# Kernel optimization log

Hardware: AMD Instinct MI355X
Metric: run time of the kernel (lower is better)

Reference implementation:

```python
import jax, jax.numpy as jnp
import numpy as np

B, C, H, W = 2, 256, 100, 100
G, P = 4, 8
CG = C // G  # 64 per-group channels
EPS = 1e-5


def setup_inputs() -> dict:
    key = jax.random.key(0)
    ks = jax.random.split(key, 5)
    bev_query = jax.random.normal(ks[0], (B, C, H, W), dtype=jnp.float32)
    pts = jax.random.normal(ks[1], (B, H * W, 1, P, C), dtype=jnp.float32)
    conv_w = jax.random.normal(ks[2], (G * CG * CG, C), dtype=jnp.float32) * (1.0 / np.sqrt(C))
    conv_b = jax.random.normal(ks[3], (G * CG * CG,), dtype=jnp.float32) * 0.02
    ln_g = jnp.ones((CG,), dtype=jnp.float32)
    ln_b = jnp.zeros((CG,), dtype=jnp.float32)
    proj_w = jax.random.normal(ks[4], (CG, CG * P), dtype=jnp.float32) * (1.0 / np.sqrt(CG * P))
    proj_b = jnp.zeros((CG,), dtype=jnp.float32)
    return {"bev_query": bev_query, "pts": pts, "conv_w": conv_w, "conv_b": conv_b,
            "ln_g": ln_g, "ln_b": ln_b, "proj_w": proj_w, "proj_b": proj_b}


def reference(bev_query, pts, conv_w, conv_b, ln_g, ln_b, proj_w, proj_b):
    b, c, h, w = bev_query.shape
    q = h * w
    # pts: b q 1 p c -> b q p c
    pts = jnp.squeeze(pts, axis=2)
    # 1x1 conv parameter generator: b c h w -> b (g c1 c2) h w
    param = jnp.einsum('bchw,oc->bohw', bev_query, conv_w) + conv_b[None, :, None, None]
    # 'b (g c1 c2) h w -> (b g) (h w) c1 c2'
    param = param.reshape(b, G, CG, CG, q).transpose(0, 1, 4, 2, 3).reshape(b * G, q, CG, CG)
    # 'b q p (g c) -> (b g) q p c'
    pts_g = pts.reshape(b, q, P, G, CG).transpose(0, 3, 1, 2, 4).reshape(b * G, q, P, CG)
    # batched per-pixel matmul: (bg,q,p,c1) @ (bg,q,c1,c2) -> (bg,q,p,c2)
    mixed = jnp.matmul(pts_g, param)
    # LayerNorm over last dim + ReLU
    mu = jnp.mean(mixed, axis=-1, keepdims=True)
    var = jnp.var(mixed, axis=-1, keepdims=True)
    normed = (mixed - mu) * jax.lax.rsqrt(var + EPS) * ln_g + ln_b
    act = jax.nn.relu(normed)
    # 'b q p c -> b q (p c)' then linear
    flat = act.reshape(b * G, q, P * CG)
    out = jnp.einsum('bqi,oi->bqo', flat, proj_w) + proj_b
    # '(b g) (h w) c -> b (g c) h w'
    out = out.reshape(b, G, q, CG).transpose(0, 1, 3, 2).reshape(b, G * CG, h, w)
    return out
```

## Files before the change

### kernel.cpp

```cpp
#include <hip/hip_runtime.h>
#include <hip/hip_bf16.h>
#include <stdint.h>

#define QTOT 10000
#define MPAD 10240
#define CDIM 256
#define ODIM 16384
#define RTOT 20096

using f32x4  = __attribute__((ext_vector_type(4))) float;
using bf16x8 = __attribute__((ext_vector_type(8))) short;

#define GLOAD_LDS(gp, lp) __builtin_amdgcn_global_load_lds(                     \
    (const __attribute__((address_space(1))) unsigned int*)(gp),                \
    (__attribute__((address_space(3))) unsigned int*)(lp), 16, 0, 0)

static __device__ __forceinline__ short f2bs(float x) {
  __hip_bfloat16 h = __float2bfloat16(x);
  return *(short*)&h;
}

__global__ void cvt_f32_bf16(const float* __restrict__ s, __hip_bfloat16* __restrict__ d, int n) {
  for (int i = blockIdx.x * blockDim.x + threadIdx.x; i < n; i += gridDim.x * blockDim.x)
    d[i] = __float2bfloat16(s[i]);
}

__global__ void cvt_permute_cw(const float* __restrict__ s, __hip_bfloat16* __restrict__ d, int n) {
  for (int i = blockIdx.x * blockDim.x + threadIdx.x; i < n; i += gridDim.x * blockDim.x) {
    int rn = i >> 8, c = i & 255;
    int ro = (rn & ~4095) | ((rn & 63) << 6) | ((rn >> 6) & 63);
    d[i] = __float2bfloat16(s[ro * 256 + c]);
  }
}

__global__ __launch_bounds__(256) void transpose_bev(const float* __restrict__ bev,
                                                     __hip_bfloat16* __restrict__ bevT) {
  __shared__ float tl[32][33];
  int tx = threadIdx.x, ty = threadIdx.y;
  int q0 = blockIdx.x * 32, c0 = blockIdx.y * 32, b = blockIdx.z;
#pragma unroll
  for (int i = 0; i < 4; ++i) {
    int c = c0 + ty + i * 8, q = q0 + tx;
    tl[ty + i * 8][tx] = (q < QTOT) ? bev[((size_t)b * CDIM + c) * QTOT + q] : 0.0f;
  }
  __syncthreads();
#pragma unroll
  for (int i = 0; i < 4; ++i) {
    int q = q0 + ty + i * 8, c = c0 + tx;
    bevT[((size_t)b * MPAD + q) * CDIM + c] = __float2bfloat16(tl[tx][ty + i * 8]);
  }
}

__global__ __launch_bounds__(256) void gemm_param(const __hip_bfloat16* __restrict__ A,
                                                  const __hip_bfloat16* __restrict__ Bw,
                                                  const float* __restrict__ convb,
                                                  __hip_bfloat16* __restrict__ P,
                                                  int nbm) {
  __shared__ __align__(16) unsigned char smem[65536];
  int t = threadIdx.x, lane = t & 63, w = t >> 6;
  int id = blockIdx.x + nbm * blockIdx.y;
  int total = nbm * gridDim.y;
  int nid = (total & 7) ? id : ((id & 7) * (total >> 3) + (id >> 3));
  int bm = nid % nbm, bn = nid / nbm;
  int wm = (w >> 1) * 64, wn = (w & 1) * 64;
  int l15 = lane & 15, hi = lane >> 4;
  int srow = lane >> 3;
  int kbs  = ((lane & 7) ^ srow) * 8;
  const __hip_bfloat16* pA = A  + (size_t)(bm * 128 + w * 32 + srow) * CDIM + kbs;
  const __hip_bfloat16* pB = Bw + (size_t)(bn * 128 + w * 32 + srow) * CDIM + kbs;
  f32x4 acc[4][4] = {};

#define LSA(buf) (smem + (buf) * 16384)
#define LSB(buf) (smem + 32768 + (buf) * 16384)
#define STAGE_P(buf, kt) do {                                                   \
    _Pragma("unroll")                                                           \
    for (int i = 0; i < 4; ++i) {                                               \
      GLOAD_LDS(pA + (size_t)i * 8 * CDIM + (kt), LSA(buf) + (w * 4 + i) * 1024); \
      GLOAD_LDS(pB + (size_t)i * 8 * CDIM + (kt), LSB(buf) + (w * 4 + i) * 1024); \
    } } while (0)

  STAGE_P(0, 0);
  asm volatile("s_waitcnt vmcnt(0)" ::: "memory");
  __builtin_amdgcn_s_barrier();
#pragma unroll
  for (int kt = 0; kt < 4; ++kt) {
    const int cur = kt & 1;
    if (kt < 3) STAGE_P(cur ^ 1, (kt + 1) * 64);
    __builtin_amdgcn_sched_barrier(0);
#pragma unroll
    for (int kk = 0; kk < 2; ++kk) {
      int kb = kk * 64 + (hi << 4);
      bf16x8 af[4], bfr[4];
#pragma unroll
      for (int mi = 0; mi < 4; ++mi) {
        int row = wm + mi * 16 + l15;
        af[mi] = *(const bf16x8*)(LSA(cur) + ((row * 128 + kb) ^ ((row & 7) << 4)));
      }
#pragma unroll
      for (int ni = 0; ni < 4; ++ni) {
        int row = wn + ni * 16 + l15;
        bfr[ni] = *(const bf16x8*)(LSB(cur) + ((row * 128 + kb) ^ ((row & 7) << 4)));
      }
#pragma unroll
      for (int mi = 0; mi < 4; ++mi)
#pragma unroll
        for (int ni = 0; ni < 4; ++ni)
          acc[mi][ni] = __builtin_amdgcn_mfma_f32_16x16x32_bf16(af[mi], bfr[ni], acc[mi][ni], 0, 0, 0);
    }
    __builtin_amdgcn_sched_barrier(0);
    if (kt < 3) asm volatile("s_waitcnt vmcnt(0)" ::: "memory");
    __builtin_amdgcn_s_barrier();
    __builtin_amdgcn_sched_barrier(0);
  }
  short* st = (short*)smem;
#pragma unroll
  for (int ni = 0; ni < 4; ++ni) {
    int colL = wn + ni * 16 + l15;
    int col  = bn * 128 + colL;
    int o_old = (col & ~4095) | ((col & 63) << 6) | ((col >> 6) & 63);
    float cb = convb[o_old];
#pragma unroll
    for (int mi = 0; mi < 4; ++mi) {
      int rowL = wm + mi * 16 + hi * 4;
#pragma unroll
      for (int r = 0; r < 4; ++r)
        st[(rowL + r) * 136 + colL] = f2bs(acc[mi][ni][r] + cb);
    }
  }
  __syncthreads();
  {
    int cb8  = (t & 15) * 8;
    size_t colg = bn * 128 + cb8;
    size_t rb0  = (size_t)bm * 128;
#pragma unroll
    for (int it = 0; it < 8; ++it) {
      int row = it * 16 + (t >> 4);
      uint4 v = *(const uint4*)(st + row * 136 + cb8);
      *(uint4*)(P + (rb0 + row) * ODIM + colg) = v;
    }
  }
#undef STAGE_P
#undef LSA
#undef LSB
}

__global__ __launch_bounds__(256) void mix_mfma(const __hip_bfloat16* __restrict__ P,
                                                const float* __restrict__ pts,
                                                const float* __restrict__ lng,
                                                const float* __restrict__ lnb,
                                                __hip_bfloat16* __restrict__ act,
                                                int b, int q0) {
  __shared__ __align__(16) float ptsl[8 * 264];
  int t = threadIdx.x, lane = t & 63, g = t >> 6;
  int row = blockIdx.x;
  size_t rq = (size_t)b * QTOT + q0 + row;
  {
    const float4* ps = (const float4*)(pts + rq * 2048);
#pragma unroll
    for (int i = 0; i < 2; ++i) {
      int v = i * 256 + t;
      float4 val = ps[v];
      int p = v >> 6, c = (v & 63) * 4;
      *(float4*)(ptsl + p * 264 + c) = val;
    }
  }
  __syncthreads();
  int l15 = lane & 15, hi = lane >> 4;
  bf16x8 bfr[2];
#pragma unroll
  for (int kk = 0; kk < 2; ++kk) {
    bf16x8 v = {};
    if (l15 < 8) {
      const float* src = ptsl + l15 * 264 + g * 64 + kk * 32 + hi * 8;
#pragma unroll
      for (int j = 0; j < 8; ++j) v[j] = f2bs(src[j]);
    }
    bfr[kk] = v;
  }
  const __hip_bfloat16* Ap = P + (size_t)row * ODIM + g * 4096;
  f32x4 acc[4] = {};
#pragma unroll
  for (int kk = 0; kk < 2; ++kk)
#pragma unroll
    for (int mi = 0; mi < 4; ++mi) {
      bf16x8 a = *(const bf16x8*)(Ap + (size_t)(mi * 16 + l15) * 64 + kk * 32 + hi * 8);
      acc[mi] = __builtin_amdgcn_mfma_f32_16x16x32_bf16(a, bfr[kk], acc[mi], 0, 0, 0);
    }
  float s = 0.f, ss = 0.f;
#pragma unroll
  for (int mi = 0; mi < 4; ++mi)
#pragma unroll
    for (int r = 0; r < 4; ++r) { float v = acc[mi][r]; s += v; ss = fmaf(v, v, ss); }
  s += __shfl_xor(s, 16);  ss += __shfl_xor(ss, 16);
  s += __shfl_xor(s, 32);  ss += __shfl_xor(ss, 32);
  float mu  = s * 0.015625f;
  float var = ss * 0.015625f - mu * mu;
  float rs  = rsqrtf(var + 1e-5f);
  if (l15 < 8) {
    short* ab = (short*)act + ((size_t)g * RTOT + rq) * 512 + l15 * 64;
#pragma unroll
    for (int mi = 0; mi < 4; ++mi) {
      int c2 = mi * 16 + hi * 4;
      float4 gg = *(const float4*)(lng + c2);
      float4 bb = *(const float4*)(lnb + c2);
      short4 o;
      o.x = f2bs(fmaxf(0.f, (acc[mi][0] - mu) * rs * gg.x + bb.x));
      o.y = f2bs(fmaxf(0.f, (acc[mi][1] - mu) * rs * gg.y + bb.y));
      o.z = f2bs(fmaxf(0.f, (acc[mi][2] - mu) * rs * gg.z + bb.z));
      o.w = f2bs(fmaxf(0.f, (acc[mi][3] - mu) * rs * gg.w + bb.w));
      *(short4*)(ab + c2) = o;
    }
  }
}

__global__ __launch_bounds__(256) void gemm_proj(const __hip_bfloat16* __restrict__ act,
                                                 const __hip_bfloat16* __restrict__ Bp,
                                                 const float* __restrict__ projb,
                                                 float* __restrict__ out) {
  __shared__ __align__(16) unsigned char lsA[2][16384];
  __shared__ __align__(16) unsigned char lsB[2][8192];
  int t = threadIdx.x, lane = t & 63, w = t >> 6;
  int bm = blockIdx.x, g = blockIdx.y;
  int wm = (w >> 1) * 64, wn = (w & 1) * 32;
  int srow = lane >> 3;
  int kbs  = ((lane & 7) ^ srow) * 8;
  const __hip_bfloat16* A  = act + (size_t)g * RTOT * 512;
  const __hip_bfloat16* pA = A  + (size_t)(bm * 128 + w * 32 + srow) * 512 + kbs;
  const __hip_bfloat16* pB = Bp + (size_t)(w * 16 + srow) * 512 + kbs;
  f32x4 acc[4][2] = {};

#define STAGE_Q(buf, kt) do {                                                   \
    _Pragma("unroll")                                                           \
    for (int i = 0; i < 4; ++i)                                                 \
      GLOAD_LDS(pA + (size_t)i * 8 * 512 + (kt), lsA[buf] + (w * 4 + i) * 1024); \
    _Pragma("unroll")                                                           \
    for (int j = 0; j < 2; ++j)                                                 \
      GLOAD_LDS(pB + (size_t)j * 8 * 512 + (kt), lsB[buf] + (w * 2 + j) * 1024); \
    } while (0)

  STAGE_Q(0, 0);
  asm volatile("s_waitcnt vmcnt(0)" ::: "memory");
  __builtin_amdgcn_s_barrier();
#pragma unroll
  for (int kt = 0; kt < 8; ++kt) {
    const int cur = kt & 1;
    if (kt < 7) STAGE_Q(cur ^ 1, (kt + 1) * 64);
    __builtin_amdgcn_sched_barrier(0);
#pragma unroll
    for (int kk = 0; kk < 2; ++kk) {
      int kb = kk * 64 + ((lane >> 4) << 4);
      bf16x8 af[4], bfr[2];
#pragma unroll
      for (int mi = 0; mi < 4; ++mi) {
        int row = wm + mi * 16 + (lane & 15);
        af[mi] = *(const bf16x8*)(lsA[cur] + ((row * 128 + kb) ^ ((row & 7) << 4)));
      }
#pragma unroll
      for (int ni = 0; ni < 2; ++ni) {
        int row = wn + ni * 16 + (lane & 15);
        bfr[ni] = *(const bf16x8*)(lsB[cur] + ((row * 128 + kb) ^ ((row & 7) << 4)));
      }
#pragma unroll
      for (int mi = 0; mi < 4; ++mi)
#pragma unroll
        for (int ni = 0; ni < 2; ++ni)
          acc[mi][ni] = __builtin_amdgcn_mfma_f32_16x16x32_bf16(af[mi], bfr[ni], acc[mi][ni], 0, 0, 0);
    }
    __builtin_amdgcn_sched_barrier(0);
    if (kt < 7) asm volatile("s_waitcnt vmcnt(0)" ::: "memory");
    __builtin_amdgcn_s_barrier();
    __builtin_amdgcn_sched_barrier(0);
  }
#pragma unroll
  for (int ni = 0; ni < 2; ++ni) {
    int o = wn + ni * 16 + (lane & 15);
    int c = g * 64 + o;
    float pbv = projb[o];
#pragma unroll
    for (int mi = 0; mi < 4; ++mi) {
      int rg = bm * 128 + wm + mi * 16 + ((lane >> 4) << 2);
      float4 o4;
      o4.x = acc[mi][ni][0] + pbv; o4.y = acc[mi][ni][1] + pbv;
      o4.z = acc[mi][ni][2] + pbv; o4.w = acc[mi][ni][3] + pbv;
      if (rg + 3 < QTOT) {
        *(float4*)(out + (size_t)c * QTOT + rg) = o4;
      } else if (rg >= QTOT && rg + 3 < 2 * QTOT) {
        *(float4*)(out + (size_t)(CDIM + c) * QTOT + (rg - QTOT)) = o4;
      } else {
#pragma unroll
        for (int r = 0; r < 4; ++r) {
          int q = rg + r;
          if (q < QTOT)          out[(size_t)c * QTOT + q] = (&o4.x)[r];
          else if (q < 2 * QTOT) out[(size_t)(CDIM + c) * QTOT + (q - QTOT)] = (&o4.x)[r];
        }
      }
    }
  }
#undef STAGE_Q
}

extern "C" void kernel_launch(void* const* d_in, const int* in_sizes, int n_in,
                              void* d_out, int out_size, void* d_ws, size_t ws_size,
                              hipStream_t stream) {
  const float* bev = (const float*)d_in[0];
  const float* pts = (const float*)d_in[1];
  const float* cw  = (const float*)d_in[2];
  const float* cb  = (const float*)d_in[3];
  const float* lng = (const float*)d_in[4];
  const float* lnb = (const float*)d_in[5];
  const float* pw  = (const float*)d_in[6];
  const float* pb  = (const float*)d_in[7];
  float* out = (float*)d_out;

  char* ws = (char*)d_ws;
  size_t off = 0;
  auto carve = [&](size_t bytes) -> char* {
    char* p = ws + off;
    off += (bytes + 255) & ~(size_t)255;
    return p;
  };
  __hip_bfloat16* cw_bf = (__hip_bfloat16*)carve((size_t)ODIM * CDIM * 2);
  __hip_bfloat16* bevT  = (__hip_bfloat16*)carve((size_t)2 * MPAD * CDIM * 2);
  __hip_bfloat16* pw_bf = (__hip_bfloat16*)carve((size_t)64 * 512 * 2);
  __hip_bfloat16* act   = (__hip_bfloat16*)carve((size_t)4 * RTOT * 512 * 2);
  size_t fixed = off;

  int CH = 128;
  const int ladder[4] = {2560, 1280, 640, 128};
  for (int i = 0; i < 4; ++i) {
    size_t need = fixed + (((size_t)ladder[i] * ODIM * 2 + 255) & ~(size_t)255);
    if (need <= ws_size) { CH = ladder[i]; break; }
  }
  __hip_bfloat16* param = (__hip_bfloat16*)carve((size_t)CH * ODIM * 2);

  cvt_permute_cw<<<4096, 256, 0, stream>>>(cw, cw_bf, ODIM * CDIM);
  cvt_f32_bf16<<<128, 256, 0, stream>>>(pw, pw_bf, 64 * 512);
  transpose_bev<<<dim3(MPAD / 32, CDIM / 32, 2), dim3(32, 8), 0, stream>>>(bev, bevT);

  int nbm = CH / 128;
  int nchunks = (QTOT + CH - 1) / CH;
  for (int b = 0; b < 2; ++b) {
    for (int c = 0; c < nchunks; ++c) {
      int q0 = c * CH;
      int nvalid = QTOT - q0;
      if (nvalid > CH) nvalid = CH;
      const __hip_bfloat16* Ab = bevT + ((size_t)b * MPAD + q0) * CDIM;
      gemm_param<<<dim3(nbm, ODIM / 128), 256, 0, stream>>>(Ab, cw_bf, cb, param, nbm);
      mix_mfma<<<dim3(nvalid), 256, 0, stream>>>(param, pts, lng, lnb, act, b, q0);
    }
  }
  gemm_proj<<<dim3(RTOT / 128, 4), 256, 0, stream>>>(act, pw_bf, pb, out);
}
```

Baseline: 511.0 us.

## Halve gemm_param LDS footprint with 32-wide K stages and two-pass epilogue

```diff
diff --git a/kernel.cpp b/kernel.cpp
--- a/kernel.cpp
+++ b/kernel.cpp
@@ -56,7 +56,7 @@
                                                   const float* __restrict__ convb,
                                                   __hip_bfloat16* __restrict__ P,
                                                   int nbm) {
-  __shared__ __align__(16) unsigned char smem[65536];
+  __shared__ __align__(16) unsigned char smem[32768];
   int t = threadIdx.x, lane = t & 63, w = t >> 6;
   int id = blockIdx.x + nbm * blockIdx.y;
   int total = nbm * gridDim.y;
@@ -64,42 +64,41 @@
   int bm = nid % nbm, bn = nid / nbm;
   int wm = (w >> 1) * 64, wn = (w & 1) * 64;
   int l15 = lane & 15, hi = lane >> 4;
-  int srow = lane >> 3;
-  int kbs  = ((lane & 7) ^ srow) * 8;
-  const __hip_bfloat16* pA = A  + (size_t)(bm * 128 + w * 32 + srow) * CDIM + kbs;
-  const __hip_bfloat16* pB = Bw + (size_t)(bn * 128 + w * 32 + srow) * CDIM + kbs;
+  int rs  = lane >> 2;
+  int ksw = ((lane & 3) ^ ((rs + (rs >> 2)) & 3)) * 8;
+  const __hip_bfloat16* pA = A  + (size_t)(bm * 128 + w * 32 + rs) * CDIM + ksw;
+  const __hip_bfloat16* pB = Bw + (size_t)(bn * 128 + w * 32 + rs) * CDIM + ksw;
+  int sl = (l15 + (l15 >> 2)) & 3;
   f32x4 acc[4][4] = {};
 
-#define LSA(buf) (smem + (buf) * 16384)
-#define LSB(buf) (smem + 32768 + (buf) * 16384)
+#define LSA(buf) (smem + (buf) * 8192)
+#define LSB(buf) (smem + 16384 + (buf) * 8192)
 #define STAGE_P(buf, kt) do {                                                   \
     _Pragma("unroll")                                                           \
-    for (int i = 0; i < 4; ++i) {                                               \
-      GLOAD_LDS(pA + (size_t)i * 8 * CDIM + (kt), LSA(buf) + (w * 4 + i) * 1024); \
-      GLOAD_LDS(pB + (size_t)i * 8 * CDIM + (kt), LSB(buf) + (w * 4 + i) * 1024); \
+    for (int i = 0; i < 2; ++i) {                                               \
+      GLOAD_LDS(pA + (size_t)i * 16 * CDIM + (kt), LSA(buf) + (w * 2 + i) * 1024); \
+      GLOAD_LDS(pB + (size_t)i * 16 * CDIM + (kt), LSB(buf) + (w * 2 + i) * 1024); \
     } } while (0)
 
   STAGE_P(0, 0);
   asm volatile("s_waitcnt vmcnt(0)" ::: "memory");
   __builtin_amdgcn_s_barrier();
 #pragma unroll
-  for (int kt = 0; kt < 4; ++kt) {
+  for (int kt = 0; kt < 8; ++kt) {
     const int cur = kt & 1;
-    if (kt < 3) STAGE_P(cur ^ 1, (kt + 1) * 64);
-    __builtin_amdgcn_sched_barrier(0);
-#pragma unroll
-    for (int kk = 0; kk < 2; ++kk) {
-      int kb = kk * 64 + (hi << 4);
+    if (kt < 7) STAGE_P(cur ^ 1, (kt + 1) * 32);
+    __builtin_amdgcn_sched_barrier(0);
+    {
       bf16x8 af[4], bfr[4];
 #pragma unroll
       for (int mi = 0; mi < 4; ++mi) {
-        int row = wm + mi * 16 + l15;
-        af[mi] = *(const bf16x8*)(LSA(cur) + ((row * 128 + kb) ^ ((row & 7) << 4)));
+        int slab = (wm >> 4) + mi;
+        af[mi] = *(const bf16x8*)(LSA(cur) + slab * 1024 + (l15 * 4 + (hi ^ sl)) * 16);
       }
 #pragma unroll
       for (int ni = 0; ni < 4; ++ni) {
-        int row = wn + ni * 16 + l15;
-        bfr[ni] = *(const bf16x8*)(LSB(cur) + ((row * 128 + kb) ^ ((row & 7) << 4)));
+        int slab = (wn >> 4) + ni;
+        bfr[ni] = *(const bf16x8*)(LSB(cur) + slab * 1024 + (l15 * 4 + (hi ^ sl)) * 16);
       }
 #pragma unroll
       for (int mi = 0; mi < 4; ++mi)
@@ -108,36 +107,43 @@
           acc[mi][ni] = __builtin_amdgcn_mfma_f32_16x16x32_bf16(af[mi], bfr[ni], acc[mi][ni], 0, 0, 0);
     }
     __builtin_amdgcn_sched_barrier(0);
-    if (kt < 3) asm volatile("s_waitcnt vmcnt(0)" ::: "memory");
+    if (kt < 7) asm volatile("s_waitcnt vmcnt(0)" ::: "memory");
     __builtin_amdgcn_s_barrier();
     __builtin_amdgcn_sched_barrier(0);
   }
   short* st = (short*)smem;
+  float cbv[4];
+  int colL[4];
 #pragma unroll
   for (int ni = 0; ni < 4; ++ni) {
-    int colL = wn + ni * 16 + l15;
-    int col  = bn * 128 + colL;
+    colL[ni] = wn + ni * 16 + l15;
+    int col = bn * 128 + colL[ni];
     int o_old = (col & ~4095) | ((col & 63) << 6) | ((col >> 6) & 63);
-    float cb = convb[o_old];
-#pragma unroll
-    for (int mi = 0; mi < 4; ++mi) {
-      int rowL = wm + mi * 16 + hi * 4;
-#pragma unroll
-      for (int r = 0; r < 4; ++r)
-        st[(rowL + r) * 136 + colL] = f2bs(acc[mi][ni][r] + cb);
-    }
-  }
-  __syncthreads();
-  {
-    int cb8  = (t & 15) * 8;
-    size_t colg = bn * 128 + cb8;
-    size_t rb0  = (size_t)bm * 128;
-#pragma unroll
-    for (int it = 0; it < 8; ++it) {
+    cbv[ni] = convb[o_old];
+  }
+  int cb8 = (t & 15) * 8;
+  size_t colg = (size_t)bn * 128 + cb8;
+#pragma unroll
+  for (int pass = 0; pass < 2; ++pass) {
+    if ((wm >> 6) == pass) {
+#pragma unroll
+      for (int ni = 0; ni < 4; ++ni)
+#pragma unroll
+        for (int mi = 0; mi < 4; ++mi) {
+          int rowL = mi * 16 + hi * 4;
+#pragma unroll
+          for (int r = 0; r < 4; ++r)
+            st[(rowL + r) * 136 + colL[ni]] = f2bs(acc[mi][ni][r] + cbv[ni]);
+        }
+    }
+    __syncthreads();
+#pragma unroll
+    for (int it = 0; it < 4; ++it) {
       int row = it * 16 + (t >> 4);
       uint4 v = *(const uint4*)(st + row * 136 + cb8);
-      *(uint4*)(P + (rb0 + row) * ODIM + colg) = v;
-    }
+      *(uint4*)(P + (size_t)(bm * 128 + pass * 64 + row) * ODIM + colg) = v;
+    }
+    __syncthreads();
   }
 #undef STAGE_P
 #undef LSA
```

Measured after the change: 542.0 us. 1.06x slower.

## Fuse param GEMM and mix into one launch, pipelined over double-buffered chunks

Applied to the files above, without the earlier changes.

```diff
diff --git a/kernel.cpp b/kernel.cpp
--- a/kernel.cpp
+++ b/kernel.cpp
@@ -51,24 +51,40 @@
   }
 }
 
-__global__ __launch_bounds__(256) void gemm_param(const __hip_bfloat16* __restrict__ A,
-                                                  const __hip_bfloat16* __restrict__ Bw,
-                                                  const float* __restrict__ convb,
-                                                  __hip_bfloat16* __restrict__ P,
-                                                  int nbm) {
+__global__ __launch_bounds__(256) void gemm_mix(const __hip_bfloat16* __restrict__ bevT,
+                                                const __hip_bfloat16* __restrict__ Bw,
+                                                const float* __restrict__ convb,
+                                                __hip_bfloat16* __restrict__ Pout,
+                                                const __hip_bfloat16* __restrict__ Pin,
+                                                const float* __restrict__ pts,
+                                                const float* __restrict__ lng,
+                                                const float* __restrict__ lnb,
+                                                __hip_bfloat16* __restrict__ act,
+                                                int ngemm, int nmix, int nbm,
+                                                int bg, int q0g,
+                                                int bmx, int q0m, int nvalidm) {
   __shared__ __align__(16) unsigned char smem[65536];
   int t = threadIdx.x, lane = t & 63, w = t >> 6;
-  int id = blockIdx.x + nbm * blockIdx.y;
-  int total = nbm * gridDim.y;
-  int nid = (total & 7) ? id : ((id & 7) * (total >> 3) + (id >> 3));
-  int bm = nid % nbm, bn = nid / nbm;
-  int wm = (w >> 1) * 64, wn = (w & 1) * 64;
-  int l15 = lane & 15, hi = lane >> 4;
-  int srow = lane >> 3;
-  int kbs  = ((lane & 7) ^ srow) * 8;
-  const __hip_bfloat16* pA = A  + (size_t)(bm * 128 + w * 32 + srow) * CDIM + kbs;
-  const __hip_bfloat16* pB = Bw + (size_t)(bn * 128 + w * 32 + srow) * CDIM + kbs;
-  f32x4 acc[4][4] = {};
+  int mn = ngemm < nmix ? ngemm : nmix;
+  int m2 = 2 * mn;
+  int bid = blockIdx.x;
+  bool isGemm;
+  int rid;
+  if (bid < m2) { isGemm = !(bid & 1); rid = bid >> 1; }
+  else          { isGemm = (ngemm > nmix); rid = mn + (bid - m2); }
+
+  if (isGemm) {
+    int total = ngemm;
+    int nid = (total & 7) ? rid : ((rid & 7) * (total >> 3) + (rid >> 3));
+    int bm = nid % nbm, bn = nid / nbm;
+    int wm = (w >> 1) * 64, wn = (w & 1) * 64;
+    int l15 = lane & 15, hi = lane >> 4;
+    int srow = lane >> 3;
+    int kbs  = ((lane & 7) ^ srow) * 8;
+    const __hip_bfloat16* A  = bevT + ((size_t)bg * MPAD + q0g) * CDIM;
+    const __hip_bfloat16* pA = A  + (size_t)(bm * 128 + w * 32 + srow) * CDIM + kbs;
+    const __hip_bfloat16* pB = Bw + (size_t)(bn * 128 + w * 32 + srow) * CDIM + kbs;
+    f32x4 acc[4][4] = {};
 
 #define LSA(buf) (smem + (buf) * 16384)
 #define LSB(buf) (smem + 32768 + (buf) * 16384)
@@ -79,136 +95,131 @@
       GLOAD_LDS(pB + (size_t)i * 8 * CDIM + (kt), LSB(buf) + (w * 4 + i) * 1024); \
     } } while (0)
 
-  STAGE_P(0, 0);
-  asm volatile("s_waitcnt vmcnt(0)" ::: "memory");
-  __builtin_amdgcn_s_barrier();
-#pragma unroll
-  for (int kt = 0; kt < 4; ++kt) {
-    const int cur = kt & 1;
-    if (kt < 3) STAGE_P(cur ^ 1, (kt + 1) * 64);
-    __builtin_amdgcn_sched_barrier(0);
-#pragma unroll
-    for (int kk = 0; kk < 2; ++kk) {
-      int kb = kk * 64 + (hi << 4);
-      bf16x8 af[4], bfr[4];
+    STAGE_P(0, 0);
+    asm volatile("s_waitcnt vmcnt(0)" ::: "memory");
+    __builtin_amdgcn_s_barrier();
+#pragma unroll
+    for (int kt = 0; kt < 4; ++kt) {
+      const int cur = kt & 1;
+      if (kt < 3) STAGE_P(cur ^ 1, (kt + 1) * 64);
+      __builtin_amdgcn_sched_barrier(0);
+#pragma unroll
+      for (int kk = 0; kk < 2; ++kk) {
+        int kb = kk * 64 + (hi << 4);
+        bf16x8 af[4], bfr[4];
+#pragma unroll
+        for (int mi = 0; mi < 4; ++mi) {
+          int row = wm + mi * 16 + l15;
+          af[mi] = *(const bf16x8*)(LSA(cur) + ((row * 128 + kb) ^ ((row & 7) << 4)));
+        }
+#pragma unroll
+        for (int ni = 0; ni < 4; ++ni) {
+          int row = wn + ni * 16 + l15;
+          bfr[ni] = *(const bf16x8*)(LSB(cur) + ((row * 128 + kb) ^ ((row & 7) << 4)));
+        }
+#pragma unroll
+        for (int mi = 0; mi < 4; ++mi)
+#pragma unroll
+          for (int ni = 0; ni < 4; ++ni)
+            acc[mi][ni] = __builtin_amdgcn_mfma_f32_16x16x32_bf16(af[mi], bfr[ni], acc[mi][ni], 0, 0, 0);
+      }
+      __builtin_amdgcn_sched_barrier(0);
+      if (kt < 3) asm volatile("s_waitcnt vmcnt(0)" ::: "memory");
+      __builtin_amdgcn_s_barrier();
+      __builtin_amdgcn_sched_barrier(0);
+    }
+    short* st = (short*)smem;
+#pragma unroll
+    for (int ni = 0; ni < 4; ++ni) {
+      int colL = wn + ni * 16 + l15;
+      int col  = bn * 128 + colL;
+      int o_old = (col & ~4095) | ((col & 63) << 6) | ((col >> 6) & 63);
+      float cb = convb[o_old];
 #pragma unroll
       for (int mi = 0; mi < 4; ++mi) {
-        int row = wm + mi * 16 + l15;
-        af[mi] = *(const bf16x8*)(LSA(cur) + ((row * 128 + kb) ^ ((row & 7) << 4)));
-      }
-#pragma unroll
-      for (int ni = 0; ni < 4; ++ni) {
-        int row = wn + ni * 16 + l15;
-        bfr[ni] = *(const bf16x8*)(LSB(cur) + ((row * 128 + kb) ^ ((row & 7) << 4)));
-      }
-#pragma unroll
-      for (int mi = 0; mi < 4; ++mi)
-#pragma unroll
-        for (int ni = 0; ni < 4; ++ni)
-          acc[mi][ni] = __builtin_amdgcn_mfma_f32_16x16x32_bf16(af[mi], bfr[ni], acc[mi][ni], 0, 0, 0);
-    }
-    __builtin_amdgcn_sched_barrier(0);
-    if (kt < 3) asm volatile("s_waitcnt vmcnt(0)" ::: "memory");
-    __builtin_amdgcn_s_barrier();
-    __builtin_amdgcn_sched_barrier(0);
-  }
-  short* st = (short*)smem;
-#pragma unroll
-  for (int ni = 0; ni < 4; ++ni) {
-    int colL = wn + ni * 16 + l15;
-    int col  = bn * 128 + colL;
-    int o_old = (col & ~4095) | ((col & 63) << 6) | ((col >> 6) & 63);
-    float cb = convb[o_old];
-#pragma unroll
-    for (int mi = 0; mi < 4; ++mi) {
-      int rowL = wm + mi * 16 + hi * 4;
-#pragma unroll
-      for (int r = 0; r < 4; ++r)
-        st[(rowL + r) * 136 + colL] = f2bs(acc[mi][ni][r] + cb);
-    }
-  }
-  __syncthreads();
-  {
-    int cb8  = (t & 15) * 8;
-    size_t colg = bn * 128 + cb8;
-    size_t rb0  = (size_t)bm * 128;
-#pragma unroll
-    for (int it = 0; it < 8; ++it) {
-      int row = it * 16 + (t >> 4);
-      uint4 v = *(const uint4*)(st + row * 136 + cb8);
-      *(uint4*)(P + (rb0 + row) * ODIM + colg) = v;
-    }
-  }
+        int rowL = wm + mi * 16 + hi * 4;
+#pragma unroll
+        for (int r = 0; r < 4; ++r)
+          st[(rowL + r) * 136 + colL] = f2bs(acc[mi][ni][r] + cb);
+      }
+    }
+    __syncthreads();
+    {
+      int cb8  = (t & 15) * 8;
+      size_t colg = bn * 128 + cb8;
+      size_t rb0  = (size_t)bm * 128;
+#pragma unroll
+      for (int it = 0; it < 8; ++it) {
+        int row = it * 16 + (t >> 4);
+        uint4 v = *(const uint4*)(st + row * 136 + cb8);
+        *(uint4*)(Pout + (rb0 + row) * ODIM + colg) = v;
+      }
+    }
 #undef STAGE_P
 #undef LSA
 #undef LSB
-}
-
-__global__ __launch_bounds__(256) void mix_mfma(const __hip_bfloat16* __restrict__ P,
-                                                const float* __restrict__ pts,
-                                                const float* __restrict__ lng,
-                                                const float* __restrict__ lnb,
-                                                __hip_bfloat16* __restrict__ act,
-                                                int b, int q0) {
-  __shared__ __align__(16) float ptsl[8 * 264];
-  int t = threadIdx.x, lane = t & 63, g = t >> 6;
-  int row = blockIdx.x;
-  size_t rq = (size_t)b * QTOT + q0 + row;
-  {
-    const float4* ps = (const float4*)(pts + rq * 2048);
-#pragma unroll
-    for (int i = 0; i < 2; ++i) {
-      int v = i * 256 + t;
-      float4 val = ps[v];
-      int p = v >> 6, c = (v & 63) * 4;
-      *(float4*)(ptsl + p * 264 + c) = val;
-    }
-  }
-  __syncthreads();
-  int l15 = lane & 15, hi = lane >> 4;
-  bf16x8 bfr[2];
-#pragma unroll
-  for (int kk = 0; kk < 2; ++kk) {
-    bf16x8 v = {};
+  } else {
+    int row = rid;
+    if (row >= nvalidm) return;
+    float* ptsl = (float*)smem;
+    int g = w;
+    size_t rq = (size_t)bmx * QTOT + q0m + row;
+    {
+      const float4* ps = (const float4*)(pts + rq * 2048);
+#pragma unroll
+      for (int i = 0; i < 2; ++i) {
+        int v = i * 256 + t;
+        float4 val = ps[v];
+        int p = v >> 6, c = (v & 63) * 4;
+        *(float4*)(ptsl + p * 264 + c) = val;
+      }
+    }
+    __syncthreads();
+    int l15 = lane & 15, hi = lane >> 4;
+    bf16x8 bfr[2];
+#pragma unroll
+    for (int kk = 0; kk < 2; ++kk) {
+      bf16x8 v = {};
+      if (l15 < 8) {
+        const float* src = ptsl + l15 * 264 + g * 64 + kk * 32 + hi * 8;
+#pragma unroll
+        for (int j = 0; j < 8; ++j) v[j] = f2bs(src[j]);
+      }
+      bfr[kk] = v;
+    }
+    const __hip_bfloat16* Ap = Pin + (size_t)row * ODIM + g * 4096;
+    f32x4 acc[4] = {};
+#pragma unroll
+    for (int kk = 0; kk < 2; ++kk)
+#pragma unroll
+      for (int mi = 0; mi < 4; ++mi) {
+        bf16x8 a = *(const bf16x8*)(Ap + (size_t)(mi * 16 + l15) * 64 + kk * 32 + hi * 8);
+        acc[mi] = __builtin_amdgcn_mfma_f32_16x16x32_bf16(a, bfr[kk], acc[mi], 0, 0, 0);
+      }
+    float s = 0.f, ss = 0.f;
+#pragma unroll
+    for (int mi = 0; mi < 4; ++mi)
+#pragma unroll
+      for (int r = 0; r < 4; ++r) { float v = acc[mi][r]; s += v; ss = fmaf(v, v, ss); }
+    s += __shfl_xor(s, 16);  ss += __shfl_xor(ss, 16);
+    s += __shfl_xor(s, 32);  ss += __shfl_xor(ss, 32);
+    float mu  = s * 0.015625f;
+    float var = ss * 0.015625f - mu * mu;
+    float rs  = rsqrtf(var + 1e-5f);
     if (l15 < 8) {
-      const float* src = ptsl + l15 * 264 + g * 64 + kk * 32 + hi * 8;
-#pragma unroll
-      for (int j = 0; j < 8; ++j) v[j] = f2bs(src[j]);
-    }
-    bfr[kk] = v;
-  }
-  const __hip_bfloat16* Ap = P + (size_t)row * ODIM + g * 4096;
-  f32x4 acc[4] = {};
-#pragma unroll
-  for (int kk = 0; kk < 2; ++kk)
-#pragma unroll
-    for (int mi = 0; mi < 4; ++mi) {
-      bf16x8 a = *(const bf16x8*)(Ap + (size_t)(mi * 16 + l15) * 64 + kk * 32 + hi * 8);
-      acc[mi] = __builtin_amdgcn_mfma_f32_16x16x32_bf16(a, bfr[kk], acc[mi], 0, 0, 0);
-    }
-  float s = 0.f, ss = 0.f;
-#pragma unroll
-  for (int mi = 0; mi < 4; ++mi)
-#pragma unroll
-    for (int r = 0; r < 4; ++r) { float v = acc[mi][r]; s += v; ss = fmaf(v, v, ss); }
-  s += __shfl_xor(s, 16);  ss += __shfl_xor(ss, 16);
-  s += __shfl_xor(s, 32);  ss += __shfl_xor(ss, 32);
-  float mu  = s * 0.015625f;
-  float var = ss * 0.015625f - mu * mu;
-  float rs  = rsqrtf(var + 1e-5f);
-  if (l15 < 8) {
-    short* ab = (short*)act + ((size_t)g * RTOT + rq) * 512 + l15 * 64;
-#pragma unroll
-    for (int mi = 0; mi < 4; ++mi) {
-      int c2 = mi * 16 + hi * 4;
-      float4 gg = *(const float4*)(lng + c2);
-      float4 bb = *(const float4*)(lnb + c2);
-      short4 o;
-      o.x = f2bs(fmaxf(0.f, (acc[mi][0] - mu) * rs * gg.x + bb.x));
-      o.y = f2bs(fmaxf(0.f, (acc[mi][1] - mu) * rs * gg.y + bb.y));
-      o.z = f2bs(fmaxf(0.f, (acc[mi][2] - mu) * rs * gg.z + bb.z));
-      o.w = f2bs(fmaxf(0.f, (acc[mi][3] - mu) * rs * gg.w + bb.w));
-      *(short4*)(ab + c2) = o;
+      short* ab = (short*)act + ((size_t)g * RTOT + rq) * 512 + l15 * 64;
+#pragma unroll
+      for (int mi = 0; mi < 4; ++mi) {
+        int c2 = mi * 16 + hi * 4;
+        float4 gg = *(const float4*)(lng + c2);
+        float4 bb = *(const float4*)(lnb + c2);
+        short4 o;
+        o.x = f2bs(fmaxf(0.f, (acc[mi][0] - mu) * rs * gg.x + bb.x));
+        o.y = f2bs(fmaxf(0.f, (acc[mi][1] - mu) * rs * gg.y + bb.y));
+        o.z = f2bs(fmaxf(0.f, (acc[mi][2] - mu) * rs * gg.z + bb.z));
+        o.w = f2bs(fmaxf(0.f, (acc[mi][3] - mu) * rs * gg.w + bb.w));
+        *(short4*)(ab + c2) = o;
+      }
     }
   }
 }
@@ -328,26 +339,36 @@
   int CH = 128;
   const int ladder[4] = {2560, 1280, 640, 128};
   for (int i = 0; i < 4; ++i) {
-    size_t need = fixed + (((size_t)ladder[i] * ODIM * 2 + 255) & ~(size_t)255);
+    size_t need = fixed + 2 * (((size_t)ladder[i] * ODIM * 2 + 255) & ~(size_t)255);
     if (need <= ws_size) { CH = ladder[i]; break; }
   }
-  __hip_bfloat16* param = (__hip_bfloat16*)carve((size_t)CH * ODIM * 2);
+  __hip_bfloat16* paramA = (__hip_bfloat16*)carve((size_t)CH * ODIM * 2);
+  __hip_bfloat16* paramB = (__hip_bfloat16*)carve((size_t)CH * ODIM * 2);
 
   cvt_permute_cw<<<4096, 256, 0, stream>>>(cw, cw_bf, ODIM * CDIM);
   cvt_f32_bf16<<<128, 256, 0, stream>>>(pw, pw_bf, 64 * 512);
   transpose_bev<<<dim3(MPAD / 32, CDIM / 32, 2), dim3(32, 8), 0, stream>>>(bev, bevT);
 
   int nbm = CH / 128;
+  int gemmBlocks = nbm * (ODIM / 128);
   int nchunks = (QTOT + CH - 1) / CH;
-  for (int b = 0; b < 2; ++b) {
-    for (int c = 0; c < nchunks; ++c) {
-      int q0 = c * CH;
-      int nvalid = QTOT - q0;
-      if (nvalid > CH) nvalid = CH;
-      const __hip_bfloat16* Ab = bevT + ((size_t)b * MPAD + q0) * CDIM;
-      gemm_param<<<dim3(nbm, ODIM / 128), 256, 0, stream>>>(Ab, cw_bf, cb, param, nbm);
-      mix_mfma<<<dim3(nvalid), 256, 0, stream>>>(param, pts, lng, lnb, act, b, q0);
-    }
+  int njobs = 2 * nchunks;
+  auto jb = [&](int j) { return j / nchunks; };
+  auto jq = [&](int j) { return (j % nchunks) * CH; };
+  auto jv = [&](int j) { int nv = QTOT - jq(j); return nv > CH ? CH : nv; };
+
+  for (int j = 0; j <= njobs; ++j) {
+    int ngemm = (j < njobs) ? gemmBlocks : 0;
+    int nmix  = (j > 0) ? jv(j - 1) : 0;
+    __hip_bfloat16* Pout = (j & 1) ? paramB : paramA;
+    const __hip_bfloat16* Pin = (j & 1) ? paramA : paramB;
+    int bg = 0, q0g = 0, bmx = 0, q0m = 0, nvm = 0;
+    if (j < njobs) { bg = jb(j); q0g = jq(j); }
+    if (j > 0)     { bmx = jb(j - 1); q0m = jq(j - 1); nvm = jv(j - 1); }
+    gemm_mix<<<dim3(ngemm + nmix), 256, 0, stream>>>(bevT, cw_bf, cb, Pout, Pin,
+                                                     pts, lng, lnb, act,
+                                                     ngemm, nmix, nbm,
+                                                     bg, q0g, bmx, q0m, nvm);
   }
   gemm_proj<<<dim3(RTOT / 128, 4), 256, 0, stream>>>(act, pw_bf, pb, out);
 }
```

After: 570.4 us. +11.6%, slower.
